# Kernel optimization log

Measured on AMD Instinct MI355X. Metric: run time of the kernel, lower is better.

## Reference

```python
import jax, jax.numpy as jnp
import numpy as np

CONF_THRES = 0.8
NMS_THRES = 0.4
IMG_SIZE = 416
MAX_DET = 3000
NEG = jnp.float32(-1e9)


def xywh2xyxy(b):
    cx, cy, w, h = b[..., 0], b[..., 1], b[..., 2], b[..., 3]
    return jnp.stack([cx - w / 2, cy - h / 2, cx + w / 2, cy + h / 2], axis=-1)


def iou_one_vs_all(box, boxes):
    # box [4], boxes [N,4]; matches original bbox_iou (+1 pixel convention, 1e-16 eps)
    ix1 = jnp.maximum(box[0], boxes[:, 0])
    iy1 = jnp.maximum(box[1], boxes[:, 1])
    ix2 = jnp.minimum(box[2], boxes[:, 2])
    iy2 = jnp.minimum(box[3], boxes[:, 3])
    inter = jnp.clip(ix2 - ix1 + 1, 0) * jnp.clip(iy2 - iy1 + 1, 0)
    a1 = (box[2] - box[0] + 1) * (box[3] - box[1] + 1)
    a2 = (boxes[:, 2] - boxes[:, 0] + 1) * (boxes[:, 3] - boxes[:, 1] + 1)
    return inter / (a1 + a2 - inter + 1e-16)


def nms_single(pred):
    # pred [N, 85] = [cx, cy, w, h, obj, 80 class scores]
    boxes = xywh2xyxy(pred[:, :4])
    obj = pred[:, 4]
    cls_conf = jnp.max(pred[:, 5:], axis=1)
    cls_id = jnp.argmax(pred[:, 5:], axis=1).astype(pred.dtype)
    valid = obj >= CONF_THRES
    score = jnp.where(valid, obj * cls_conf, NEG)
    order = jnp.argsort(-score)  # descending score, invalid pushed to end
    boxes, obj = boxes[order], obj[order]
    cls_conf, cls_id = cls_conf[order], cls_id[order]
    alive0 = valid[order]

    def step(alive, _):
        any_alive = jnp.any(alive)
        idx = jnp.argmax(alive)  # first surviving = highest remaining score
        iou = iou_one_vs_all(boxes[idx], boxes)
        invalid = (iou > NMS_THRES) & (cls_id == cls_id[idx]) & alive
        w = jnp.where(invalid, obj, 0.0)
        wsum = jnp.where(any_alive, w.sum(), 1.0)
        merged = (w[:, None] * boxes).sum(0) / wsum  # obj-weighted box merge, as original
        det = jnp.concatenate([merged, jnp.stack([obj[idx], cls_conf[idx], cls_id[idx]])])
        det = jnp.where(any_alive, det, NEG)
        return alive & ~invalid, (det, any_alive)

    _, (kept, kept_mask) = jax.lax.scan(step, alive0, None, length=MAX_DET)
    return kept, kept_mask  # kept [MAX_DET,7] = [x1,y1,x2,y2,obj,cls_conf,cls_id]


def setup_inputs() -> dict:
    key = jax.random.key(0)
    k1, k2, k3, k4 = jax.random.split(key, 4)
    B, N, C = 16, 10647, 80
    cxy = jax.random.uniform(k1, (B, N, 2), jnp.float32) * IMG_SIZE   # box centers in pixels
    wh = jax.random.uniform(k2, (B, N, 2), jnp.float32) * 80.0 + 2.0  # box sizes
    obj = jax.random.uniform(k3, (B, N, 1), jnp.float32)              # objectness
    cls = jax.random.uniform(k4, (B, N, C), jnp.float32)              # class scores
    return {"detections": jnp.concatenate([cxy, wh, obj, cls], axis=-1)}


def reference(detections):
    # NMS on every image (original non_max_suppression iterates whole batch)
    kept, kept_mask = jax.vmap(nms_single)(detections)
    # YoloModel.forward: take image 0, columns [class_conf, class_id],
    # sort ascending by class_conf then flip -> descending; return probs.
    conf0 = jnp.where(kept_mask[0], kept[0, :, 5], NEG)
    probs = -jnp.sort(-conf0)  # padded slots are NEG at the tail
    return probs
```

## Files before the change

### kernel.cpp

```cpp
#include <hip/hip_runtime.h>

#pragma clang fp contract(off)

#define N_BOX   10647
#define N_CLS   80
#define ROW     85
#define CONF_T  0.8f
#define NMS_T   0.4f
#define NEGV    -1000000000.0f
#define KMAX    256
#define OUT_N   3000
#define SURV_N  4096
#define NBLK    192
#define NTHR    256
#define ROWS_PB ((N_BOX + NBLK - 1) / NBLK)
#define CTR_SURV 80
#define CTR_BAR  120

#define AT_LDF(p)   __hip_atomic_load((p),  __ATOMIC_RELAXED, __HIP_MEMORY_SCOPE_AGENT)
#define AT_LDI(p)   __hip_atomic_load((p),  __ATOMIC_RELAXED, __HIP_MEMORY_SCOPE_AGENT)
#define AT_STF(p,v) __hip_atomic_store((p), (v), __ATOMIC_RELAXED, __HIP_MEMORY_SCOPE_AGENT)
#define AT_STI(p,v) __hip_atomic_store((p), (v), __ATOMIC_RELAXED, __HIP_MEMORY_SCOPE_AGENT)

__device__ __forceinline__ void grid_bar(int* bar, int target) {
    __syncthreads();
    if (threadIdx.x == 0) {
        __builtin_amdgcn_s_waitcnt(0);
        __hip_atomic_fetch_add(bar, 1, __ATOMIC_RELAXED, __HIP_MEMORY_SCOPE_AGENT);
        long guard = 0;
        while (__hip_atomic_load(bar, __ATOMIC_RELAXED, __HIP_MEMORY_SCOPE_AGENT) < target) {
            __builtin_amdgcn_s_sleep(2);
            if (++guard > (1L << 26)) break;
        }
    }
    __syncthreads();
}

__global__ __launch_bounds__(NTHR) void k_fused(const float* __restrict__ det,
                                                float* __restrict__ out,
                                                int* counters,
                                                float* bx1, float* by1,
                                                float* bx2, float* by2,
                                                float* bsc, float* bcf, int* bix,
                                                float* surv) {
    __shared__ float lds[ROWS_PB * ROW];
    __shared__ int nkeep, base;
    const int tid  = threadIdx.x;
    const int bid  = blockIdx.x;
    const int gidx = bid * NTHR + tid;
    int* bar = counters + CTR_BAR;

    {
        const int row0 = bid * ROWS_PB;
        int nrows = N_BOX - row0; if (nrows > ROWS_PB) nrows = ROWS_PB;
        if (nrows > 0) {
            const int nflt = nrows * ROW;
            const float* src = det + (size_t)row0 * ROW;
            const int n4 = nflt >> 2;
            float4* l4 = (float4*)lds;
            const float4* s4 = (const float4*)src;
            for (int j = tid; j < n4; j += NTHR) l4[j] = s4[j];
            for (int j = (n4 << 2) + tid; j < nflt; j += NTHR) lds[j] = src[j];
            __syncthreads();
            if (tid < nrows) {
                const float* p = lds + tid * ROW;
                float obj = p[4];
                if (obj >= CONF_T) {
                    float cx = p[0], cy = p[1], w = p[2], h = p[3];
                    float hw = w / 2.0f, hh = h / 2.0f;
                    float best = p[5]; int bcls = 0;
                    for (int c = 1; c < N_CLS; ++c) {
                        float v = p[5 + c];
                        if (v > best) { best = v; bcls = c; }
                    }
                    int pos = atomicAdd(&counters[bcls], 1);
                    if (pos < KMAX) {
                        int o = bcls * KMAX + pos;
                        AT_STF(&bx1[o], cx - hw); AT_STF(&by1[o], cy - hh);
                        AT_STF(&bx2[o], cx + hw); AT_STF(&by2[o], cy + hh);
                        AT_STF(&bsc[o], obj * best); AT_STF(&bcf[o], best);
                        AT_STI(&bix[o], row0 + tid);
                    }
                }
            }
        }
    }
    grid_bar(bar, NBLK);

    if (bid < N_CLS) {
        float* rsc   = lds;
        int*   ridx  = (int*)(lds + KMAX);
        float* sx1   = lds + 2 * KMAX;
        float* sy1   = lds + 3 * KMAX;
        float* sx2   = lds + 4 * KMAX;
        float* sy2   = lds + 5 * KMAX;
        float* scf   = lds + 6 * KMAX;
        float* keepc = lds + 7 * KMAX;
        unsigned char* alive = (unsigned char*)(lds + 8 * KMAX);

        const int c = bid;
        if (tid == 0) nkeep = 0;
        int k = AT_LDI(&counters[c]); if (k > KMAX) k = KMAX;

        for (int i = tid; i < k; i += NTHR) {
            rsc[i] = AT_LDF(&bsc[c * KMAX + i]);
            ridx[i] = AT_LDI(&bix[c * KMAX + i]);
        }
        __syncthreads();

        for (int i = tid; i < k; i += NTHR) {
            float s = rsc[i]; int id = ridx[i]; int r = 0;
            for (int j = 0; j < k; ++j) {
                float sj = rsc[j];
                r += (sj > s) || (sj == s && ridx[j] < id);
            }
            int o = c * KMAX + i;
            sx1[r] = AT_LDF(&bx1[o]); sy1[r] = AT_LDF(&by1[o]);
            sx2[r] = AT_LDF(&bx2[o]); sy2[r] = AT_LDF(&by2[o]);
            scf[r] = AT_LDF(&bcf[o]);
            alive[r] = 1;
        }
        __syncthreads();

        for (int i = 0; i < k; ++i) {
            bool a = (alive[i] != 0);
            __syncthreads();
            if (a) {
                if (tid == 0) { keepc[nkeep++] = scf[i]; alive[i] = 0; }
                float px1 = sx1[i], py1 = sy1[i], px2 = sx2[i], py2 = sy2[i];
                float a1 = ((px2 - px1) + 1.0f) * ((py2 - py1) + 1.0f);
                for (int j = i + 1 + tid; j < k; j += NTHR) {
                    if (!alive[j]) continue;
                    float ix1 = fmaxf(px1, sx1[j]);
                    float iy1 = fmaxf(py1, sy1[j]);
                    float ix2 = fminf(px2, sx2[j]);
                    float iy2 = fminf(py2, sy2[j]);
                    float iw = fmaxf((ix2 - ix1) + 1.0f, 0.0f);
                    float ih = fmaxf((iy2 - iy1) + 1.0f, 0.0f);
                    float inter = iw * ih;
                    float a2 = ((sx2[j] - sx1[j]) + 1.0f) * ((sy2[j] - sy1[j]) + 1.0f);
                    float den = ((a1 + a2) - inter) + 1e-16f;
                    if (inter / den > NMS_T) alive[j] = 0;
                }
            }
            __syncthreads();
        }

        if (tid == 0) base = atomicAdd(&counters[CTR_SURV], nkeep);
        __syncthreads();
        int nb = nkeep, b = base;
        for (int i = tid; i < nb; i += NTHR) {
            int o = b + i;
            if (o < SURV_N) AT_STF(&surv[o], keepc[i]);
        }
    }
    grid_bar(bar, 2 * NBLK);

    {
        int m = AT_LDI(&counters[CTR_SURV]); if (m > SURV_N) m = SURV_N;
        float* slds = lds;
        for (int i = tid; i < m; i += NTHR) slds[i] = AT_LDF(&surv[i]);
        __syncthreads();

        const int lane = tid & 63;
        const int wid  = gidx >> 6;
        for (int g = wid; g < m; g += NBLK * (NTHR / 64)) {
            const float v = slds[g];
            int cnt = 0;
            for (int j = lane; j < m; j += 64) {
                float sj = slds[j];
                cnt += (sj > v) || (sj == v && j < g);
            }
            #pragma unroll
            for (int off = 32; off > 0; off >>= 1) cnt += __shfl_down(cnt, off, 64);
            if (lane == 0 && cnt < OUT_N) out[cnt] = v;
        }
        for (int i = m + gidx; i < OUT_N; i += NBLK * NTHR) out[i] = NEGV;
    }
}

extern "C" void kernel_launch(void* const* d_in, const int* in_sizes, int n_in,
                              void* d_out, int out_size, void* d_ws, size_t ws_size,
                              hipStream_t stream) {
    const float* det = (const float*)d_in[0];
    float* out = (float*)d_out;

    const size_t NB = (size_t)N_CLS * KMAX;
    char* p = (char*)d_ws;
    int*   counters = (int*)p;        p += 512;
    float* bx1 = (float*)p;           p += NB * 4;
    float* by1 = (float*)p;           p += NB * 4;
    float* bx2 = (float*)p;           p += NB * 4;
    float* by2 = (float*)p;           p += NB * 4;
    float* bsc = (float*)p;           p += NB * 4;
    float* bcf = (float*)p;           p += NB * 4;
    int*   bix = (int*)p;             p += NB * 4;
    float* surv = (float*)p;

    hipMemsetAsync(d_ws, 0, 512, stream);
    hipLaunchKernelGGL(k_fused, dim3(NBLK), dim3(NTHR), 0, stream,
                       det, out, counters,
                       bx1, by1, bx2, by2, bsc, bcf, bix, surv);
}
```

Measured before the change: 49.15 us.

## Pack per-class box buffers into 64-bit words, pad counters, shrink grid to 80 blocks

```diff
diff --git a/kernel.cpp b/kernel.cpp
--- a/kernel.cpp
+++ b/kernel.cpp
@@ -11,16 +11,33 @@
 #define KMAX    256
 #define OUT_N   3000
 #define SURV_N  4096
-#define NBLK    192
+#define NBLK    80
 #define NTHR    256
-#define ROWS_PB ((N_BOX + NBLK - 1) / NBLK)
-#define CTR_SURV 80
-#define CTR_BAR  120
-
-#define AT_LDF(p)   __hip_atomic_load((p),  __ATOMIC_RELAXED, __HIP_MEMORY_SCOPE_AGENT)
-#define AT_LDI(p)   __hip_atomic_load((p),  __ATOMIC_RELAXED, __HIP_MEMORY_SCOPE_AGENT)
-#define AT_STF(p,v) __hip_atomic_store((p), (v), __ATOMIC_RELAXED, __HIP_MEMORY_SCOPE_AGENT)
-#define AT_STI(p,v) __hip_atomic_store((p), (v), __ATOMIC_RELAXED, __HIP_MEMORY_SCOPE_AGENT)
+#define ROWS_PB 136
+#define CTR_STRIDE 32
+#define CTR_SURV (80 * CTR_STRIDE)
+#define CTR_BAR  (81 * CTR_STRIDE)
+#define CTR_BYTES (82 * 128)
+
+typedef unsigned long long u64;
+typedef unsigned int u32;
+
+#define AT_LD64(p)   __hip_atomic_load((p),  __ATOMIC_RELAXED, __HIP_MEMORY_SCOPE_AGENT)
+#define AT_ST64(p,v) __hip_atomic_store((p), (v), __ATOMIC_RELAXED, __HIP_MEMORY_SCOPE_AGENT)
+#define AT_LD32(p)   __hip_atomic_load((p),  __ATOMIC_RELAXED, __HIP_MEMORY_SCOPE_AGENT)
+#define AT_ST32(p,v) __hip_atomic_store((p), (v), __ATOMIC_RELAXED, __HIP_MEMORY_SCOPE_AGENT)
+#define AT_LDF(p)    __hip_atomic_load((p),  __ATOMIC_RELAXED, __HIP_MEMORY_SCOPE_AGENT)
+#define AT_STF(p,v)  __hip_atomic_store((p), (v), __ATOMIC_RELAXED, __HIP_MEMORY_SCOPE_AGENT)
+
+__device__ __forceinline__ u64 pack_ff(float a, float b) {
+    union { float f[2]; u64 u; } x; x.f[0] = a; x.f[1] = b; return x.u;
+}
+__device__ __forceinline__ u64 pack_fi(float a, int b) {
+    union { struct { float f; int i; } s; u64 u; } x; x.s.f = a; x.s.i = b; return x.u;
+}
+__device__ __forceinline__ float lo_f(u64 v) { union { u64 u; float f[2]; } x; x.u = v; return x.f[0]; }
+__device__ __forceinline__ float hi_f(u64 v) { union { u64 u; float f[2]; } x; x.u = v; return x.f[1]; }
+__device__ __forceinline__ int   hi_i(u64 v) { union { u64 u; int i[2]; } x; x.u = v; return x.i[1]; }
 
 __device__ __forceinline__ void grid_bar(int* bar, int target) {
     __syncthreads();
@@ -39,9 +56,7 @@
 __global__ __launch_bounds__(NTHR) void k_fused(const float* __restrict__ det,
                                                 float* __restrict__ out,
                                                 int* counters,
-                                                float* bx1, float* by1,
-                                                float* bx2, float* by2,
-                                                float* bsc, float* bcf, int* bix,
+                                                u64* pA, u64* pB, u64* pS, u32* pC,
                                                 float* surv) {
     __shared__ float lds[ROWS_PB * ROW];
     __shared__ int nkeep, base;
@@ -52,13 +67,15 @@
 
     {
         const int row0 = bid * ROWS_PB;
-        int nrows = N_BOX - row0; if (nrows > ROWS_PB) nrows = ROWS_PB;
+        int nrows = N_BOX - row0;
+        if (nrows > ROWS_PB) nrows = ROWS_PB;
         if (nrows > 0) {
             const int nflt = nrows * ROW;
             const float* src = det + (size_t)row0 * ROW;
             const int n4 = nflt >> 2;
             float4* l4 = (float4*)lds;
             const float4* s4 = (const float4*)src;
+            #pragma unroll 4
             for (int j = tid; j < n4; j += NTHR) l4[j] = s4[j];
             for (int j = (n4 << 2) + tid; j < nflt; j += NTHR) lds[j] = src[j];
             __syncthreads();
@@ -73,13 +90,13 @@
                         float v = p[5 + c];
                         if (v > best) { best = v; bcls = c; }
                     }
-                    int pos = atomicAdd(&counters[bcls], 1);
+                    int pos = atomicAdd(&counters[bcls * CTR_STRIDE], 1);
                     if (pos < KMAX) {
                         int o = bcls * KMAX + pos;
-                        AT_STF(&bx1[o], cx - hw); AT_STF(&by1[o], cy - hh);
-                        AT_STF(&bx2[o], cx + hw); AT_STF(&by2[o], cy + hh);
-                        AT_STF(&bsc[o], obj * best); AT_STF(&bcf[o], best);
-                        AT_STI(&bix[o], row0 + tid);
+                        AT_ST64(&pA[o], pack_ff(cx - hw, cy - hh));
+                        AT_ST64(&pB[o], pack_ff(cx + hw, cy + hh));
+                        AT_ST64(&pS[o], pack_fi(obj * best, row0 + tid));
+                        AT_ST32(&pC[o], __float_as_uint(best));
                     }
                 }
             }
@@ -87,7 +104,7 @@
     }
     grid_bar(bar, NBLK);
 
-    if (bid < N_CLS) {
+    {
         float* rsc   = lds;
         int*   ridx  = (int*)(lds + KMAX);
         float* sx1   = lds + 2 * KMAX;
@@ -100,11 +117,12 @@
 
         const int c = bid;
         if (tid == 0) nkeep = 0;
-        int k = AT_LDI(&counters[c]); if (k > KMAX) k = KMAX;
+        int k = AT_LD32((u32*)&counters[c * CTR_STRIDE]);
+        if (k > KMAX) k = KMAX;
 
         for (int i = tid; i < k; i += NTHR) {
-            rsc[i] = AT_LDF(&bsc[c * KMAX + i]);
-            ridx[i] = AT_LDI(&bix[c * KMAX + i]);
+            u64 si = AT_LD64(&pS[c * KMAX + i]);
+            rsc[i] = lo_f(si); ridx[i] = hi_i(si);
         }
         __syncthreads();
 
@@ -115,9 +133,11 @@
                 r += (sj > s) || (sj == s && ridx[j] < id);
             }
             int o = c * KMAX + i;
-            sx1[r] = AT_LDF(&bx1[o]); sy1[r] = AT_LDF(&by1[o]);
-            sx2[r] = AT_LDF(&bx2[o]); sy2[r] = AT_LDF(&by2[o]);
-            scf[r] = AT_LDF(&bcf[o]);
+            u64 a = AT_LD64(&pA[o]);
+            u64 b = AT_LD64(&pB[o]);
+            sx1[r] = lo_f(a); sy1[r] = hi_f(a);
+            sx2[r] = lo_f(b); sy2[r] = hi_f(b);
+            scf[r] = __uint_as_float(AT_LD32(&pC[o]));
             alive[r] = 1;
         }
         __syncthreads();
@@ -157,7 +177,7 @@
     grid_bar(bar, 2 * NBLK);
 
     {
-        int m = AT_LDI(&counters[CTR_SURV]); if (m > SURV_N) m = SURV_N;
+        int m = AT_LD32((u32*)&counters[CTR_SURV]); if (m > SURV_N) m = SURV_N;
         float* slds = lds;
         for (int i = tid; i < m; i += NTHR) slds[i] = AT_LDF(&surv[i]);
         __syncthreads();
@@ -187,18 +207,14 @@
 
     const size_t NB = (size_t)N_CLS * KMAX;
     char* p = (char*)d_ws;
-    int*   counters = (int*)p;        p += 512;
-    float* bx1 = (float*)p;           p += NB * 4;
-    float* by1 = (float*)p;           p += NB * 4;
-    float* bx2 = (float*)p;           p += NB * 4;
-    float* by2 = (float*)p;           p += NB * 4;
-    float* bsc = (float*)p;           p += NB * 4;
-    float* bcf = (float*)p;           p += NB * 4;
-    int*   bix = (int*)p;             p += NB * 4;
+    int*   counters = (int*)p;  p += 16384;
+    u64*   pA   = (u64*)p;      p += NB * 8;
+    u64*   pB   = (u64*)p;      p += NB * 8;
+    u64*   pS   = (u64*)p;      p += NB * 8;
+    u32*   pC   = (u32*)p;      p += NB * 4;
     float* surv = (float*)p;
 
-    hipMemsetAsync(d_ws, 0, 512, stream);
+    hipMemsetAsync(d_ws, 0, CTR_BYTES, stream);
     hipLaunchKernelGGL(k_fused, dim3(NBLK), dim3(NTHR), 0, stream,
-                       det, out, counters,
-                       bx1, by1, bx2, by2, bsc, bcf, bix, surv);
-}
+                       det, out, counters, pA, pB, pS, pC, surv);
+}
```

After: 48.30 us, median of 4. Within noise of the previous version (-1.7%).
